# Kernel tuning notes

Measured on AMD Instinct MI355X. Metric: run time of the kernel, lower is better.

The kernel has to match this reference:

```python
import jax, jax.numpy as jnp
import numpy as np

N, E = 50000, 1600000
IN_DIM, HID, L, H = 300, 256, 3, 4
HD = HID // H  # 64
EPS = 1e-5


def setup_inputs() -> dict:
    key = jax.random.key(0)
    ks = jax.random.split(key, 24)
    s = 0.02
    inp = {
        'node_feats': jax.random.normal(ks[0], (N, IN_DIM), jnp.float32),
        'role': jax.random.randint(ks[1], (N,), 0, 3),
        'edge_src': jax.random.randint(ks[2], (E,), 0, N),
        'edge_dst': jax.random.randint(ks[3], (E,), 0, N),
        'edge_weights': jax.random.uniform(ks[4], (E,), jnp.float32),
        # input role transforms (question / entity / context)
        'Wq': jax.random.normal(ks[5], (IN_DIM, HID), jnp.float32) * s,
        'bq': jnp.zeros((HID,), jnp.float32),
        'We': jax.random.normal(ks[6], (IN_DIM, HID), jnp.float32) * s,
        'be': jnp.zeros((HID,), jnp.float32),
        'Wc': jax.random.normal(ks[7], (IN_DIM, HID), jnp.float32) * s,
        'bc': jnp.zeros((HID,), jnp.float32),
        # per-head value projections [H, HID, HD] (q/k projections omitted:
        # softmax over a scalar == 1.0, so they never affect output or grads)
        'Wv': jax.random.normal(ks[8], (H, HID, HD), jnp.float32) * s,
        'bv': jnp.zeros((H, HD), jnp.float32),
        # shared 'default' edge-type transform (the torch code always falls
        # through to 'default' because edata['rel'] entries are tensors)
        'Wd': jax.random.normal(ks[9], (HD, HD), jnp.float32) * s,
        'bd': jnp.zeros((HD,), jnp.float32),
        # attention_output
        'Wo': jax.random.normal(ks[10], (HID, HID), jnp.float32) * s,
        'bo': jnp.zeros((HID,), jnp.float32),
        # GRUCell params (torch layout: [3*HID, in], gate order r,z,n)
        'W_ih': jax.random.normal(ks[11], (3 * HID, HID), jnp.float32) * s,
        'W_hh': jax.random.normal(ks[12], (3 * HID, HID), jnp.float32) * s,
        'b_ih': jnp.zeros((3 * HID,), jnp.float32),
        'b_hh': jnp.zeros((3 * HID,), jnp.float32),
        # per-layer LayerNorm affine params [L, HID]
        'ln_w': jnp.ones((L, HID), jnp.float32),
        'ln_b': jnp.zeros((L, HID), jnp.float32),
    }
    return inp


def _layernorm(x, w, b):
    mu = jnp.mean(x, -1, keepdims=True)
    var = jnp.mean(jnp.square(x - mu), -1, keepdims=True)
    return (x - mu) * jax.lax.rsqrt(var + EPS) * w + b


def _gru_cell(x, hprev, W_ih, W_hh, b_ih, b_hh):
    gi = x @ W_ih.T + b_ih
    gh = hprev @ W_hh.T + b_hh
    i_r, i_z, i_n = jnp.split(gi, 3, axis=-1)
    h_r, h_z, h_n = jnp.split(gh, 3, axis=-1)
    r = jax.nn.sigmoid(i_r + h_r)
    z = jax.nn.sigmoid(i_z + h_z)
    n = jnp.tanh(i_n + r * h_n)
    return (1.0 - z) * n + z * hprev


def reference(node_feats, role, edge_src, edge_dst, edge_weights,
              Wq, bq, We, be, Wc, bc, Wv, bv, Wd, bd, Wo, bo,
              W_ih, W_hh, b_ih, b_hh, ln_w, ln_b):
    n_nodes = node_feats.shape[0]
    # role-dependent input transform: 0=question, 1=evidence/answer, 2=other
    hq = node_feats @ Wq + bq
    he = node_feats @ We + be
    hc = node_feats @ Wc + bc
    r = role[:, None]
    h = jax.nn.relu(jnp.where(r == 0, hq, jnp.where(r == 1, he, hc)))

    path_mem = jax.lax.stop_gradient(h)  # .detach().clone()
    prev_h = h
    num_layers, num_heads = ln_w.shape[0], Wv.shape[0]
    for layer in range(num_layers):
        head_msgs = []
        for hd in range(num_heads):
            # value proj + shared 'default' edge transform (node-level, fused)
            vt = (h @ Wv[hd] + bv[hd]) @ Wd + bd  # [N, HD]
            # scalar softmax == 1.0 -> attn_weight == edge_weight
            msg = vt[edge_src] * edge_weights[:, None]  # [E, HD]
            head_msgs.append(jax.ops.segment_sum(msg, edge_dst,
                                                 num_segments=n_nodes))
        combined = jnp.concatenate(head_msgs, axis=-1)  # [N, HID]
        path_mem = _gru_cell(combined, path_mem, W_ih, W_hh, b_ih, b_hh)
        h = _layernorm(prev_h + combined @ Wo + bo, ln_w[layer], ln_b[layer])
        # dropout: identity in eval mode
        prev_h = h
    return h + path_mem
```

## Files before the change

kernel.cpp:

```cpp
#include <hip/hip_runtime.h>
#include <math.h>

#define NN 50000
#define EE 1600000
#define IND 300
#define KPAD 320
#define NL 3
#define NBLK 785
#define AGG_NB 12500

typedef unsigned short u16;
typedef __attribute__((ext_vector_type(8))) short short8;
typedef __attribute__((ext_vector_type(4))) float floatx4;

__device__ __forceinline__ float b2f(u16 u) {
  union { unsigned i; float f; } v; v.i = ((unsigned)u) << 16; return v.f;
}
__device__ __forceinline__ u16 f2b(float f) {
  union { unsigned i; float f; } v; v.f = f;
  unsigned b = v.i; b += 0x7fffu + ((b >> 16) & 1u);
  return (u16)(b >> 16);
}
__device__ __forceinline__ float sigf(float x) { return 1.0f / (1.0f + __expf(-x)); }

__global__ void count_kernel(const int* __restrict__ dst, int* __restrict__ cnt) {
  int e = blockIdx.x * 256 + threadIdx.x;
  if (e < EE) atomicAdd(&cnt[dst[e]], 1);
}

__global__ __launch_bounds__(256) void scan1_kernel(const int* __restrict__ cnt,
                                                    int* __restrict__ rs,
                                                    int* __restrict__ bsum) {
  __shared__ int ws[4];
  const int t = threadIdx.x, l = t & 63, w = t >> 6;
  const int base = blockIdx.x * 2048 + t * 8;
  int v[8];
  int tot = 0;
  #pragma unroll
  for (int k = 0; k < 8; ++k) {
    int i = base + k;
    v[k] = (i < NN) ? cnt[i] : 0;
    tot += v[k];
  }
  int x = tot;
  #pragma unroll
  for (int off = 1; off < 64; off <<= 1) {
    int y = __shfl_up(x, off);
    if (l >= off) x += y;
  }
  if (l == 63) ws[w] = x;
  __syncthreads();
  int wpre = 0;
  for (int q = 0; q < w; ++q) wpre += ws[q];
  int run = wpre + (x - tot);
  #pragma unroll
  for (int k = 0; k < 8; ++k) {
    int i = base + k;
    if (i < NN) rs[i] = run;
    run += v[k];
  }
  if (t == 255) bsum[blockIdx.x] = wpre + x;
}

__global__ void scan2_kernel(int* __restrict__ bsum, int nb) {
  int l = threadIdx.x;
  int v = (l < nb) ? bsum[l] : 0;
  int x = v;
  #pragma unroll
  for (int off = 1; off < 64; off <<= 1) {
    int y = __shfl_up(x, off);
    if (l >= off) x += y;
  }
  if (l < nb) bsum[l] = x - v;
  if (l == 63) bsum[nb] = x;
}

__global__ void scan3_kernel(const int* __restrict__ bsum, int* __restrict__ rs, int nb) {
  int i = blockIdx.x * 256 + threadIdx.x;
  if (i < NN) rs[i] += bsum[i >> 11];
  if (i == 0) rs[NN] = bsum[nb];
}

__global__ void fill_kernel(const int* __restrict__ dst, const int* __restrict__ rs,
                            int* __restrict__ ncnt, const int* __restrict__ esrc,
                            const float* __restrict__ ew, int2* __restrict__ srcw) {
  int e = blockIdx.x * 256 + threadIdx.x;
  if (e < EE) {
    int d = dst[e];
    int p = atomicAdd(&ncnt[d], 1);
    int2 v;
    v.x = esrc[e];
    v.y = __float_as_int(ew[e]);
    srcw[rs[d] + p] = v;
  }
}

__global__ void role_count(const int* __restrict__ role, int* __restrict__ cnt3) {
  __shared__ int lc[3];
  if (threadIdx.x < 3) lc[threadIdx.x] = 0;
  __syncthreads();
  int i = blockIdx.x * 256 + threadIdx.x;
  if (i < NN) atomicAdd(&lc[role[i]], 1);
  __syncthreads();
  if (threadIdx.x < 3) atomicAdd(&cnt3[threadIdx.x], lc[threadIdx.x]);
}

__global__ void role_plan(const int* __restrict__ cnt3, int* __restrict__ pbase,
                          int* __restrict__ blkrole) {
  __shared__ int pb[4];
  if (threadIdx.x == 0) {
    pb[0] = 0;
    for (int b = 0; b < 3; ++b) pb[b + 1] = pb[b] + (((cnt3[b] + 63) >> 6) << 6);
    for (int b = 0; b < 4; ++b) pbase[b] = pb[b];
  }
  __syncthreads();
  for (int blk = threadIdx.x; blk < NBLK; blk += 256) {
    int m0 = blk * 64;
    int r = -1;
    for (int b = 0; b < 3; ++b)
      if (m0 >= pb[b] && m0 < pb[b + 1]) r = b;
    blkrole[blk] = r;
  }
}

__global__ void role_fill(const int* __restrict__ role, const int* __restrict__ pbase,
                          int* __restrict__ pos3, int* __restrict__ perm) {
  __shared__ int lcnt[3], lbase[3];
  int i = blockIdx.x * 256 + threadIdx.x;
  if (threadIdx.x < 3) lcnt[threadIdx.x] = 0;
  __syncthreads();
  int r = 0, lr = 0;
  bool valid = (i < NN);
  if (valid) {
    r = role[i];
    lr = atomicAdd(&lcnt[r], 1);
  }
  __syncthreads();
  if (threadIdx.x < 3) lbase[threadIdx.x] = atomicAdd(&pos3[threadIdx.x], lcnt[threadIdx.x]);
  __syncthreads();
  if (valid) perm[pbase[r] + lbase[r] + lr] = i;
}

__global__ void xcast_kernel(const float* __restrict__ X, u16* __restrict__ Xb) {
  size_t i = (size_t)blockIdx.x * 256 + threadIdx.x;
  if (i >= (size_t)NN * KPAD) return;
  int r = (int)(i / KPAD), k = (int)(i % KPAD);
  Xb[i] = (k < IND) ? f2b(X[(size_t)r * IND + k]) : (u16)0;
}

__global__ void wt3_kernel(const float* __restrict__ Wq, const float* __restrict__ We,
                           const float* __restrict__ Wc, u16* __restrict__ Wqt,
                           u16* __restrict__ Wet, u16* __restrict__ Wct) {
  int n = blockIdx.x;
  int which = blockIdx.y;
  const float* W = (which == 0) ? Wq : (which == 1) ? We : Wc;
  u16* Wt = (which == 0) ? Wqt : (which == 1) ? Wet : Wct;
  for (int k = threadIdx.x; k < KPAD; k += 256)
    Wt[(size_t)n * KPAD + k] = (k < IND) ? f2b(W[(size_t)k * 256 + n]) : (u16)0;
}

__global__ void wallt_kernel(const float* __restrict__ Wv, const float* __restrict__ Wd,
                             u16* __restrict__ Wallt) {
  int i = blockIdx.x;
  int c = threadIdx.x;
  int hd = c >> 6, j = c & 63;
  const float* wv = &Wv[hd * (256 * 64) + i * 64];
  float s = 0.f;
  #pragma unroll
  for (int m = 0; m < 64; ++m) s = fmaf(wv[m], Wd[m * 64 + j], s);
  Wallt[(size_t)c * 256 + i] = f2b(s);
}

__global__ void ball_kernel(const float* __restrict__ bv, const float* __restrict__ Wd,
                            const float* __restrict__ bd, float* __restrict__ ball) {
  int c = threadIdx.x;
  int hd = c >> 6, j = c & 63;
  float s = bd[j];
  #pragma unroll
  for (int m = 0; m < 64; ++m) s = fmaf(bv[hd * 64 + m], Wd[m * 64 + j], s);
  ball[c] = s;
}

__global__ void wot_kernel(const float* __restrict__ Wo, u16* __restrict__ Wot) {
  int n = blockIdx.x;
  int k = threadIdx.x;
  Wot[(size_t)n * 256 + k] = f2b(Wo[(size_t)k * 256 + n]);
}

__global__ void castbf2_kernel(const float* __restrict__ s0, const float* __restrict__ s1,
                               u16* __restrict__ d0, u16* __restrict__ d1) {
  int i = blockIdx.x * 256 + threadIdx.x;
  const int n = 768 * 256;
  if (i < n) d0[i] = f2b(s0[i]);
  else if (i < 2 * n) d1[i - n] = f2b(s1[i - n]);
}

#define GEMM_PROLOG \
  __shared__ __align__(16) u16 As[64][72]; \
  __shared__ __align__(16) u16 Bs[64][72]; \
  const int t = threadIdx.x; \
  const int lane = t & 63; \
  const int wv_ = t >> 6; \
  const int wr = wv_ >> 1, wc = wv_ & 1; \
  const int l15 = lane & 15, l4 = lane >> 4; \
  const int srow = t >> 2; \
  const int scol = (t & 3) << 4;

#define STAGE_A(AG, ASTRIDE, VALID, ROWIDX, K0) { \
  int4 v0 = {0, 0, 0, 0}, v1 = {0, 0, 0, 0}; \
  if (VALID) { \
    const int4* p_ = (const int4*)&(AG)[(size_t)(ROWIDX) * (ASTRIDE) + (K0) + scol]; \
    v0 = p_[0]; v1 = p_[1]; \
  } \
  *(int4*)&As[srow][scol] = v0; \
  *(int4*)&As[srow][scol + 8] = v1; }

#define STAGE_B(BG, BSTRIDE, ROWIDX, K0) { \
  const int4* p_ = (const int4*)&(BG)[(size_t)(ROWIDX) * (BSTRIDE) + (K0) + scol]; \
  *(int4*)&Bs[srow][scol] = p_[0]; \
  *(int4*)&Bs[srow][scol + 8] = p_[1]; }

#define MFMA_STEP(ACC) { \
  _Pragma("unroll") \
  for (int kc = 0; kc < 2; ++kc) { \
    short8 a0_ = *(const short8*)&As[wr * 32 + 0 + l15][kc * 32 + l4 * 8]; \
    short8 a1_ = *(const short8*)&As[wr * 32 + 16 + l15][kc * 32 + l4 * 8]; \
    short8 b0_ = *(const short8*)&Bs[wc * 32 + 0 + l15][kc * 32 + l4 * 8]; \
    short8 b1_ = *(const short8*)&Bs[wc * 32 + 16 + l15][kc * 32 + l4 * 8]; \
    ACC[0][0] = __builtin_amdgcn_mfma_f32_16x16x32_bf16(a0_, b0_, ACC[0][0], 0, 0, 0); \
    ACC[0][1] = __builtin_amdgcn_mfma_f32_16x16x32_bf16(a0_, b1_, ACC[0][1], 0, 0, 0); \
    ACC[1][0] = __builtin_amdgcn_mfma_f32_16x16x32_bf16(a1_, b0_, ACC[1][0], 0, 0, 0); \
    ACC[1][1] = __builtin_amdgcn_mfma_f32_16x16x32_bf16(a1_, b1_, ACC[1][1], 0, 0, 0); \
  } }

#define GEMM128_PROLOG \
  __shared__ __align__(16) u16 As[128][72]; \
  __shared__ __align__(16) u16 Bs[128][72]; \
  const int t = threadIdx.x; \
  const int lane = t & 63; \
  const int wv_ = t >> 6; \
  const int qr = (wv_ >> 1) * 64, qc = (wv_ & 1) * 64; \
  const int l15 = lane & 15, l4 = lane >> 4; \
  const int srow = t >> 1; \
  const int scol = (t & 1) * 32;

#define STAGE128_A(AG, ASTRIDE, VALID, ROWIDX, K0) { \
  int4 v0 = {0,0,0,0}, v1 = {0,0,0,0}, v2 = {0,0,0,0}, v3 = {0,0,0,0}; \
  if (VALID) { \
    const int4* p_ = (const int4*)&(AG)[(size_t)(ROWIDX) * (ASTRIDE) + (K0) + scol]; \
    v0 = p_[0]; v1 = p_[1]; v2 = p_[2]; v3 = p_[3]; \
  } \
  *(int4*)&As[srow][scol] = v0; *(int4*)&As[srow][scol + 8] = v1; \
  *(int4*)&As[srow][scol + 16] = v2; *(int4*)&As[srow][scol + 24] = v3; }

#define STAGE128_B(BG, BSTRIDE, ROWIDX, K0) { \
  const int4* p_ = (const int4*)&(BG)[(size_t)(ROWIDX) * (BSTRIDE) + (K0) + scol]; \
  *(int4*)&Bs[srow][scol] = p_[0]; *(int4*)&Bs[srow][scol + 8] = p_[1]; \
  *(int4*)&Bs[srow][scol + 16] = p_[2]; *(int4*)&Bs[srow][scol + 24] = p_[3]; }

#define MFMA128_STEP(ACC) { \
  _Pragma("unroll") \
  for (int kc = 0; kc < 2; ++kc) { \
    short8 af_[4], bf_[4]; \
    _Pragma("unroll") \
    for (int m = 0; m < 4; ++m) af_[m] = *(const short8*)&As[qr + m * 16 + l15][kc * 32 + l4 * 8]; \
    _Pragma("unroll") \
    for (int n = 0; n < 4; ++n) bf_[n] = *(const short8*)&Bs[qc + n * 16 + l15][kc * 32 + l4 * 8]; \
    _Pragma("unroll") \
    for (int m = 0; m < 4; ++m) \
      _Pragma("unroll") \
      for (int n = 0; n < 4; ++n) \
        ACC[m][n] = __builtin_amdgcn_mfma_f32_16x16x32_bf16(af_[m], bf_[n], ACC[m][n], 0, 0, 0); \
  } }

__global__ __launch_bounds__(256) void proj_mfma(
    const u16* __restrict__ Xb, const int* __restrict__ perm,
    const int* __restrict__ blkrole,
    const u16* __restrict__ Wqt, const u16* __restrict__ Wet, const u16* __restrict__ Wct,
    const float* __restrict__ bq, const float* __restrict__ be, const float* __restrict__ bc,
    u16* __restrict__ h, u16* __restrict__ pm) {
  const int brole = blkrole[blockIdx.y];
  if (brole < 0) return;
  GEMM_PROLOG
  const int m0 = blockIdx.y * 64;
  const int n0 = blockIdx.x * 64;
  const u16* Bt = (brole == 0) ? Wqt : (brole == 1) ? Wet : Wct;
  const float* bb = (brole == 0) ? bq : (brole == 1) ? be : bc;
  const int prow = perm[m0 + srow];
  floatx4 acc[2][2] = {};
  for (int k0 = 0; k0 < KPAD; k0 += 64) {
    STAGE_A(Xb, KPAD, prow >= 0, prow, k0)
    STAGE_B(Bt, KPAD, n0 + srow, k0)
    __syncthreads();
    MFMA_STEP(acc)
    __syncthreads();
  }
  #pragma unroll
  for (int m = 0; m < 2; ++m)
    #pragma unroll
    for (int reg = 0; reg < 4; ++reg) {
      int gr = m0 + wr * 32 + m * 16 + l4 * 4 + reg;
      int pr = perm[gr];
      if (pr >= 0) {
        #pragma unroll
        for (int n = 0; n < 2; ++n) {
          int c = n0 + wc * 32 + n * 16 + l15;
          float vo = fmaxf(acc[m][n][reg] + bb[c], 0.f);
          u16 ub = f2b(vo);
          h[(size_t)pr * 256 + c] = ub;
          pm[(size_t)pr * 256 + c] = ub;
        }
      }
    }
}

__global__ __launch_bounds__(256) void vgemm_mfma(
    const u16* __restrict__ A, const u16* __restrict__ Bt,
    const float* __restrict__ bias, u16* __restrict__ C) {
  GEMM128_PROLOG
  const int m0 = blockIdx.y * 128;
  const int n0 = blockIdx.x * 128;
  const int ar = m0 + srow;
  floatx4 acc[4][4] = {};
  for (int k0 = 0; k0 < 256; k0 += 64) {
    STAGE128_A(A, 256, ar < NN, ar, k0)
    STAGE128_B(Bt, 256, n0 + srow, k0)
    __syncthreads();
    MFMA128_STEP(acc)
    __syncthreads();
  }
  #pragma unroll
  for (int m = 0; m < 4; ++m)
    #pragma unroll
    for (int reg = 0; reg < 4; ++reg) {
      int gr = m0 + qr + m * 16 + l4 * 4 + reg;
      if (gr < NN) {
        #pragma unroll
        for (int n = 0; n < 4; ++n) {
          int c = n0 + qc + n * 16 + l15;
          C[(size_t)gr * 256 + c] = f2b(acc[m][n][reg] + bias[c]);
        }
      }
    }
}

__global__ __launch_bounds__(256) void agg_kernel(
    const int2* __restrict__ srcw, const int* __restrict__ rs,
    const u16* __restrict__ V, u16* __restrict__ comb) {
  int bid = blockIdx.x;
  int slice = (bid >= AGG_NB) ? 1 : 0;
  int nb = bid - slice * AGG_NB;
  int n = nb * 4 + (threadIdx.x >> 6);
  int l = threadIdx.x & 63;
  if (n >= NN) return;
  int s = rs[n], e = rs[n + 1];
  const size_t coff = (size_t)(slice << 7) + l * 2;
  float a0 = 0.f, a1 = 0.f, c0 = 0.f, c1 = 0.f;
  for (int base = s; base < e; base += 64) {
    int2 p = {0, 0};
    if (base + l < e) p = srcw[base + l];
    int cnt = min(64, e - base);
    int j = 0;
    for (; j + 4 <= cnt; j += 4) {
      int s0 = __shfl(p.x, j + 0), s1 = __shfl(p.x, j + 1);
      int s2 = __shfl(p.x, j + 2), s3 = __shfl(p.x, j + 3);
      float w0 = __int_as_float(__shfl(p.y, j + 0));
      float w1 = __int_as_float(__shfl(p.y, j + 1));
      float w2 = __int_as_float(__shfl(p.y, j + 2));
      float w3 = __int_as_float(__shfl(p.y, j + 3));
      ushort2 v0 = *(const ushort2*)&V[(size_t)s0 * 256 + coff];
      ushort2 v1 = *(const ushort2*)&V[(size_t)s1 * 256 + coff];
      ushort2 v2 = *(const ushort2*)&V[(size_t)s2 * 256 + coff];
      ushort2 v3 = *(const ushort2*)&V[(size_t)s3 * 256 + coff];
      a0 = fmaf(w0, b2f(v0.x), a0); a1 = fmaf(w0, b2f(v0.y), a1);
      c0 = fmaf(w1, b2f(v1.x), c0); c1 = fmaf(w1, b2f(v1.y), c1);
      a0 = fmaf(w2, b2f(v2.x), a0); a1 = fmaf(w2, b2f(v2.y), a1);
      c0 = fmaf(w3, b2f(v3.x), c0); c1 = fmaf(w3, b2f(v3.y), c1);
    }
    for (; j < cnt; ++j) {
      int src = __shfl(p.x, j);
      float w = __int_as_float(__shfl(p.y, j));
      ushort2 v = *(const ushort2*)&V[(size_t)src * 256 + coff];
      a0 = fmaf(w, b2f(v.x), a0); a1 = fmaf(w, b2f(v.y), a1);
    }
  }
  a0 += c0; a1 += c1;
  ushort2 o;
  o.x = f2b(a0); o.y = f2b(a1);
  *(ushort2*)&comb[(size_t)n * 256 + coff] = o;
}

__global__ __launch_bounds__(256) void gru_mfma(
    const u16* __restrict__ comb, const u16* __restrict__ pmc,
    const u16* __restrict__ Wiht, const u16* __restrict__ Whht,
    const float* __restrict__ bih, const float* __restrict__ bhh,
    u16* __restrict__ pmn) {
  __shared__ __align__(16) u16 As[2][64][40];
  __shared__ __align__(16) u16 Bs[6][64][40];
  const int t = threadIdx.x;
  const int lane = t & 63;
  const int wv_ = t >> 6;
  const int wr = wv_ >> 1, wc = wv_ & 1;
  const int l15 = lane & 15, l4 = lane >> 4;
  const int srow = t >> 2;
  const int kq = (t & 3) << 3;
  const int m0 = blockIdx.y * 64;
  const int cb = blockIdx.x;
  const int ar = m0 + srow;
  const bool av = ar < NN;
  floatx4 acc[6][2][2] = {};
  for (int k0 = 0; k0 < 256; k0 += 32) {
    {
      int4 v0 = {0, 0, 0, 0}, u0 = {0, 0, 0, 0};
      if (av) {
        v0 = *(const int4*)&comb[(size_t)ar * 256 + k0 + kq];
        u0 = *(const int4*)&pmc[(size_t)ar * 256 + k0 + kq];
      }
      *(int4*)&As[0][srow][kq] = v0;
      *(int4*)&As[1][srow][kq] = u0;
    }
    #pragma unroll
    for (int g = 0; g < 3; ++g) {
      size_t row = (size_t)(g * 256 + cb * 64 + srow);
      *(int4*)&Bs[g][srow][kq] = *(const int4*)&Wiht[row * 256 + k0 + kq];
      *(int4*)&Bs[3 + g][srow][kq] = *(const int4*)&Whht[row * 256 + k0 + kq];
    }
    __syncthreads();
    short8 a0f[2], a1f[2];
    #pragma unroll
    for (int m = 0; m < 2; ++m) {
      a0f[m] = *(const short8*)&As[0][wr * 32 + m * 16 + l15][l4 * 8];
      a1f[m] = *(const short8*)&As[1][wr * 32 + m * 16 + l15][l4 * 8];
    }
    #pragma unroll
    for (int g = 0; g < 3; ++g) {
      short8 b0 = *(const short8*)&Bs[g][wc * 32 + 0 + l15][l4 * 8];
      short8 b1 = *(const short8*)&Bs[g][wc * 32 + 16 + l15][l4 * 8];
      acc[g][0][0] = __builtin_amdgcn_mfma_f32_16x16x32_bf16(a0f[0], b0, acc[g][0][0], 0, 0, 0);
      acc[g][0][1] = __builtin_amdgcn_mfma_f32_16x16x32_bf16(a0f[0], b1, acc[g][0][1], 0, 0, 0);
      acc[g][1][0] = __builtin_amdgcn_mfma_f32_16x16x32_bf16(a0f[1], b0, acc[g][1][0], 0, 0, 0);
      acc[g][1][1] = __builtin_amdgcn_mfma_f32_16x16x32_bf16(a0f[1], b1, acc[g][1][1], 0, 0, 0);
    }
    #pragma unroll
    for (int g = 3; g < 6; ++g) {
      short8 b0 = *(const short8*)&Bs[g][wc * 32 + 0 + l15][l4 * 8];
      short8 b1 = *(const short8*)&Bs[g][wc * 32 + 16 + l15][l4 * 8];
      acc[g][0][0] = __builtin_amdgcn_mfma_f32_16x16x32_bf16(a1f[0], b0, acc[g][0][0], 0, 0, 0);
      acc[g][0][1] = __builtin_amdgcn_mfma_f32_16x16x32_bf16(a1f[0], b1, acc[g][0][1], 0, 0, 0);
      acc[g][1][0] = __builtin_amdgcn_mfma_f32_16x16x32_bf16(a1f[1], b0, acc[g][1][0], 0, 0, 0);
      acc[g][1][1] = __builtin_amdgcn_mfma_f32_16x16x32_bf16(a1f[1], b1, acc[g][1][1], 0, 0, 0);
    }
    __syncthreads();
  }
  #pragma unroll
  for (int m = 0; m < 2; ++m)
    #pragma unroll
    for (int reg = 0; reg < 4; ++reg) {
      int gr = m0 + wr * 32 + m * 16 + l4 * 4 + reg;
      if (gr < NN) {
        #pragma unroll
        for (int n = 0; n < 2; ++n) {
          int c = cb * 64 + wc * 32 + n * 16 + l15;
          float r = sigf(acc[0][m][n][reg] + acc[3][m][n][reg] + bih[c] + bhh[c]);
          float z = sigf(acc[1][m][n][reg] + acc[4][m][n][reg] + bih[256 + c] + bhh[256 + c]);
          float i_n = acc[2][m][n][reg] + bih[512 + c];
          float h_n = acc[5][m][n][reg] + bhh[512 + c];
          float nn2 = tanhf(i_n + r * h_n);
          float po = b2f(pmc[(size_t)gr * 256 + c]);
          pmn[(size_t)gr * 256 + c] = f2b((1.f - z) * nn2 + z * po);
        }
      }
    }
}

__global__ __launch_bounds__(256) void wo_ln_mfma(
    const u16* __restrict__ comb, const u16* __restrict__ Wot,
    const float* __restrict__ bo, const u16* __restrict__ h_in,
    const float* __restrict__ lnw, const float* __restrict__ lnb,
    u16* __restrict__ h_out, const u16* __restrict__ pm,
    float* __restrict__ out, int last) {
  __shared__ __align__(16) u16 As[64][72];
  __shared__ __align__(16) u16 Bs[256][72];
  __shared__ float2 red[64][4];
  const int t = threadIdx.x;
  const int lane = t & 63;
  const int w = t >> 6;
  const int l15 = lane & 15, l4 = lane >> 4;
  const int m0 = blockIdx.x * 64;
  const int arow = t >> 2;
  const int ascol = (t & 3) << 4;
  floatx4 acc[4][4] = {};
  for (int k0 = 0; k0 < 256; k0 += 64) {
    {
      int r = m0 + arow;
      int4 v0 = {0, 0, 0, 0}, v1 = {0, 0, 0, 0};
      if (r < NN) {
        const int4* p = (const int4*)&comb[(size_t)r * 256 + k0 + ascol];
        v0 = p[0]; v1 = p[1];
      }
      *(int4*)&As[arow][ascol] = v0;
      *(int4*)&As[arow][ascol + 8] = v1;
    }
    {
      const int4* p = (const int4*)&Wot[(size_t)t * 256 + k0];
      #pragma unroll
      for (int q = 0; q < 8; ++q) *(int4*)&Bs[t][q * 8] = p[q];
    }
    __syncthreads();
    #pragma unroll
    for (int kc = 0; kc < 2; ++kc) {
      short8 af[4], bf[4];
      #pragma unroll
      for (int m = 0; m < 4; ++m) af[m] = *(const short8*)&As[m * 16 + l15][kc * 32 + l4 * 8];
      #pragma unroll
      for (int n = 0; n < 4; ++n) bf[n] = *(const short8*)&Bs[w * 64 + n * 16 + l15][kc * 32 + l4 * 8];
      #pragma unroll
      for (int m = 0; m < 4; ++m)
        #pragma unroll
        for (int n = 0; n < 4; ++n)
          acc[m][n] = __builtin_amdgcn_mfma_f32_16x16x32_bf16(af[m], bf[n], acc[m][n], 0, 0, 0);
    }
    __syncthreads();
  }
  #pragma unroll
  for (int m = 0; m < 4; ++m)
    #pragma unroll
    for (int reg = 0; reg < 4; ++reg) {
      int rloc = m * 16 + l4 * 4 + reg;
      int gr = m0 + rloc;
      float s = 0.f, s2 = 0.f;
      #pragma unroll
      for (int n = 0; n < 4; ++n) {
        int c = w * 64 + n * 16 + l15;
        float hv = (gr < NN) ? b2f(h_in[(size_t)gr * 256 + c]) : 0.f;
        float v = acc[m][n][reg] + bo[c] + hv;
        acc[m][n][reg] = v;
        s += v;
        s2 = fmaf(v, v, s2);
      }
      #pragma unroll
      for (int off = 1; off < 16; off <<= 1) {
        s += __shfl_xor(s, off);
        s2 += __shfl_xor(s2, off);
      }
      if (l15 == 0) red[rloc][w] = make_float2(s, s2);
    }
  __syncthreads();
  #pragma unroll
  for (int m = 0; m < 4; ++m)
    #pragma unroll
    for (int reg = 0; reg < 4; ++reg) {
      int rloc = m * 16 + l4 * 4 + reg;
      int gr = m0 + rloc;
      float2 r0 = red[rloc][0], r1 = red[rloc][1], r2 = red[rloc][2], r3 = red[rloc][3];
      float tot = (r0.x + r1.x) + (r2.x + r3.x);
      float tot2 = (r0.y + r1.y) + (r2.y + r3.y);
      float mu = tot * (1.f / 256.f);
      float var = tot2 * (1.f / 256.f) - mu * mu;
      float inv = rsqrtf(fmaxf(var, 0.f) + 1e-5f);
      if (gr < NN) {
        #pragma unroll
        for (int n = 0; n < 4; ++n) {
          int c = w * 64 + n * 16 + l15;
          float lnv = (acc[m][n][reg] - mu) * inv * lnw[c] + lnb[c];
          if (last) {
            out[(size_t)gr * 256 + c] = b2f(f2b(lnv)) + b2f(pm[(size_t)gr * 256 + c]);
          } else {
            h_out[(size_t)gr * 256 + c] = f2b(lnv);
          }
        }
      }
    }
}

extern "C" void kernel_launch(void* const* d_in, const int* in_sizes, int n_in,
                              void* d_out, int out_size, void* d_ws, size_t ws_size,
                              hipStream_t stream) {
  const float* node_feats = (const float*)d_in[0];
  const int* role = (const int*)d_in[1];
  const int* esrc = (const int*)d_in[2];
  const int* edst = (const int*)d_in[3];
  const float* ew = (const float*)d_in[4];
  const float* Wq = (const float*)d_in[5];
  const float* bq = (const float*)d_in[6];
  const float* We = (const float*)d_in[7];
  const float* be = (const float*)d_in[8];
  const float* Wc = (const float*)d_in[9];
  const float* bc = (const float*)d_in[10];
  const float* Wv = (const float*)d_in[11];
  const float* bv = (const float*)d_in[12];
  const float* Wd = (const float*)d_in[13];
  const float* bd = (const float*)d_in[14];
  const float* Wo = (const float*)d_in[15];
  const float* bo = (const float*)d_in[16];
  const float* Wih = (const float*)d_in[17];
  const float* Whh = (const float*)d_in[18];
  const float* bih = (const float*)d_in[19];
  const float* bhh = (const float*)d_in[20];
  const float* lnw = (const float*)d_in[21];
  const float* lnb = (const float*)d_in[22];
  float* out = (float*)d_out;

  char* ws = (char*)d_ws;
  size_t off = 0;
  auto take = [&](size_t bytes) {
    char* p = ws + off;
    off = (off + bytes + 511) & ~(size_t)511;
    return p;
  };
  const size_t NC2 = (size_t)NN * 256 * 2;
  u16* Xb = (u16*)take((size_t)NN * KPAD * 2);
  u16* h = (u16*)take(NC2);
  u16* pm0 = (u16*)take(NC2);
  u16* pm1 = (u16*)take(NC2);
  u16* V = (u16*)take(NC2);
  u16* comb = (u16*)take(NC2);
  u16* Wqt = (u16*)take((size_t)256 * KPAD * 2);
  u16* Wet = (u16*)take((size_t)256 * KPAD * 2);
  u16* Wct = (u16*)take((size_t)256 * KPAD * 2);
  u16* Wallt = (u16*)take((size_t)256 * 256 * 2);
  u16* Wot = (u16*)take((size_t)256 * 256 * 2);
  u16* Wiht = (u16*)take((size_t)768 * 256 * 2);
  u16* Whht = (u16*)take((size_t)768 * 256 * 2);
  float* ball = (float*)take(256 * 4);
  int* cnt = (int*)take((size_t)NN * 4);
  int* rs = (int*)take((size_t)(NN + 1) * 4);
  int* ncnt = (int*)take((size_t)NN * 4);
  int2* srcw = (int2*)take((size_t)EE * 8);
  int* cnt3 = (int*)take(16);
  int* pos3 = (int*)take(16);
  int* pbase = (int*)take(16);
  int* blkrole = (int*)take((size_t)NBLK * 4);
  int* perm = (int*)take((size_t)NBLK * 64 * 4);
  int* bsum = (int*)take(64 * 4);

  const int NB_SCAN = (NN + 2047) / 2048;

  hipMemsetAsync(cnt, 0, (size_t)NN * 4, stream);
  hipMemsetAsync(ncnt, 0, (size_t)NN * 4, stream);
  hipMemsetAsync(cnt3, 0, 16, stream);
  hipMemsetAsync(pos3, 0, 16, stream);
  hipMemsetAsync(perm, 0xFF, (size_t)NBLK * 64 * 4, stream);

  count_kernel<<<(EE + 255) / 256, 256, 0, stream>>>(edst, cnt);
  scan1_kernel<<<NB_SCAN, 256, 0, stream>>>(cnt, rs, bsum);
  scan2_kernel<<<1, 64, 0, stream>>>(bsum, NB_SCAN);
  scan3_kernel<<<(NN + 255) / 256, 256, 0, stream>>>(bsum, rs, NB_SCAN);
  fill_kernel<<<(EE + 255) / 256, 256, 0, stream>>>(edst, rs, ncnt, esrc, ew, srcw);

  role_count<<<(NN + 255) / 256, 256, 0, stream>>>(role, cnt3);
  role_plan<<<1, 256, 0, stream>>>(cnt3, pbase, blkrole);
  role_fill<<<(NN + 255) / 256, 256, 0, stream>>>(role, pbase, pos3, perm);

  xcast_kernel<<<(int)(((size_t)NN * KPAD + 255) / 256), 256, 0, stream>>>(node_feats, Xb);
  wt3_kernel<<<dim3(256, 3), 256, 0, stream>>>(Wq, We, Wc, Wqt, Wet, Wct);
  wallt_kernel<<<256, 256, 0, stream>>>(Wv, Wd, Wallt);
  ball_kernel<<<1, 256, 0, stream>>>(bv, Wd, bd, ball);
  wot_kernel<<<256, 256, 0, stream>>>(Wo, Wot);
  castbf2_kernel<<<(2 * 768 * 256 + 255) / 256, 256, 0, stream>>>(Wih, Whh, Wiht, Whht);

  proj_mfma<<<dim3(4, NBLK), 256, 0, stream>>>(Xb, perm, blkrole, Wqt, Wet, Wct,
                                               bq, be, bc, h, pm0);

  u16* pmc = pm0;
  u16* pmn = pm1;
  const int MB128 = (NN + 127) / 128;
  const int MB64 = (NN + 63) / 64;
  for (int layer = 0; layer < NL; ++layer) {
    vgemm_mfma<<<dim3(2, MB128), 256, 0, stream>>>(h, Wallt, ball, V);
    agg_kernel<<<2 * AGG_NB, 256, 0, stream>>>(srcw, rs, V, comb);
    gru_mfma<<<dim3(4, MB64), 256, 0, stream>>>(comb, pmc, Wiht, Whht, bih, bhh, pmn);
    wo_ln_mfma<<<MB64, 256, 0, stream>>>(comb, Wot, bo, h,
                                         lnw + layer * 256, lnb + layer * 256,
                                         h, pmn, out, (layer == NL - 1) ? 1 : 0);
    u16* sw = pmc; pmc = pmn; pmn = sw;
  }
}
```

Baseline: 1.169 ms.

## Slice V into 32-column slabs, pack edge metadata, widen GRU K-tile

The value GEMM now writes V as eight column-major slabs of 32 columns. Aggregation then runs over eight column slices, each gathering from a much smaller slab that can stay cache-resident, with half-waves processing alternating edges through shared-memory metadata. Edge source and weight are packed into one u32 (16-bit source index, bf16 weight), which halves the metadata footprint but rounds the weights to bf16 and relies on N < 65536. Metadata is now re-read once per slice, eight times in total. The GRU GEMM also doubles its K tile to 64 to halve the number of barriers.

```diff
diff --git a/kernel.cpp b/kernel.cpp
--- a/kernel.cpp
+++ b/kernel.cpp
@@ -10,6 +10,7 @@
 #define AGG_NB 12500
 
 typedef unsigned short u16;
+typedef unsigned int u32;
 typedef __attribute__((ext_vector_type(8))) short short8;
 typedef __attribute__((ext_vector_type(4))) float floatx4;
 
@@ -83,14 +84,12 @@
 
 __global__ void fill_kernel(const int* __restrict__ dst, const int* __restrict__ rs,
                             int* __restrict__ ncnt, const int* __restrict__ esrc,
-                            const float* __restrict__ ew, int2* __restrict__ srcw) {
+                            const float* __restrict__ ew, u32* __restrict__ srcw) {
   int e = blockIdx.x * 256 + threadIdx.x;
   if (e < EE) {
     int d = dst[e];
     int p = atomicAdd(&ncnt[d], 1);
-    int2 v;
-    v.x = esrc[e];
-    v.y = __float_as_int(ew[e]);
+    u32 v = ((u32)f2b(ew[e]) << 16) | (u32)esrc[e];
     srcw[rs[d] + p] = v;
   }
 }
@@ -316,7 +315,7 @@
 
 __global__ __launch_bounds__(256) void vgemm_mfma(
     const u16* __restrict__ A, const u16* __restrict__ Bt,
-    const float* __restrict__ bias, u16* __restrict__ C) {
+    const float* __restrict__ bias, u16* __restrict__ Vs) {
   GEMM128_PROLOG
   const int m0 = blockIdx.y * 128;
   const int n0 = blockIdx.x * 128;
@@ -338,56 +337,53 @@
         #pragma unroll
         for (int n = 0; n < 4; ++n) {
           int c = n0 + qc + n * 16 + l15;
-          C[(size_t)gr * 256 + c] = f2b(acc[m][n][reg] + bias[c]);
+          size_t off = ((size_t)(c >> 5) * NN + gr) * 32 + (c & 31);
+          Vs[off] = f2b(acc[m][n][reg] + bias[c]);
         }
       }
     }
 }
 
 __global__ __launch_bounds__(256) void agg_kernel(
-    const int2* __restrict__ srcw, const int* __restrict__ rs,
-    const u16* __restrict__ V, u16* __restrict__ comb) {
+    const u32* __restrict__ srcw, const int* __restrict__ rs,
+    const u16* __restrict__ Vs, u16* __restrict__ comb) {
+  __shared__ u32 meta[4][64];
   int bid = blockIdx.x;
-  int slice = (bid >= AGG_NB) ? 1 : 0;
+  int slice = bid / AGG_NB;
   int nb = bid - slice * AGG_NB;
-  int n = nb * 4 + (threadIdx.x >> 6);
-  int l = threadIdx.x & 63;
-  if (n >= NN) return;
+  int wid = threadIdx.x >> 6;
+  int n = nb * 4 + wid;
+  int lane = threadIdx.x & 63;
+  int hh = lane >> 5;
+  int u = lane & 31;
   int s = rs[n], e = rs[n + 1];
-  const size_t coff = (size_t)(slice << 7) + l * 2;
-  float a0 = 0.f, a1 = 0.f, c0 = 0.f, c1 = 0.f;
+  const u16* __restrict__ vbase = Vs + (size_t)slice * NN * 32;
+  float a0 = 0.f, a1 = 0.f, a2 = 0.f, a3 = 0.f;
   for (int base = s; base < e; base += 64) {
-    int2 p = {0, 0};
-    if (base + l < e) p = srcw[base + l];
+    u32 m = 0;
+    if (base + lane < e) m = srcw[base + lane];
+    meta[wid][lane] = m;
     int cnt = min(64, e - base);
-    int j = 0;
-    for (; j + 4 <= cnt; j += 4) {
-      int s0 = __shfl(p.x, j + 0), s1 = __shfl(p.x, j + 1);
-      int s2 = __shfl(p.x, j + 2), s3 = __shfl(p.x, j + 3);
-      float w0 = __int_as_float(__shfl(p.y, j + 0));
-      float w1 = __int_as_float(__shfl(p.y, j + 1));
-      float w2 = __int_as_float(__shfl(p.y, j + 2));
-      float w3 = __int_as_float(__shfl(p.y, j + 3));
-      ushort2 v0 = *(const ushort2*)&V[(size_t)s0 * 256 + coff];
-      ushort2 v1 = *(const ushort2*)&V[(size_t)s1 * 256 + coff];
-      ushort2 v2 = *(const ushort2*)&V[(size_t)s2 * 256 + coff];
-      ushort2 v3 = *(const ushort2*)&V[(size_t)s3 * 256 + coff];
-      a0 = fmaf(w0, b2f(v0.x), a0); a1 = fmaf(w0, b2f(v0.y), a1);
-      c0 = fmaf(w1, b2f(v1.x), c0); c1 = fmaf(w1, b2f(v1.y), c1);
-      a0 = fmaf(w2, b2f(v2.x), a0); a1 = fmaf(w2, b2f(v2.y), a1);
-      c0 = fmaf(w3, b2f(v3.x), c0); c1 = fmaf(w3, b2f(v3.y), c1);
-    }
-    for (; j < cnt; ++j) {
-      int src = __shfl(p.x, j);
-      float w = __int_as_float(__shfl(p.y, j));
-      ushort2 v = *(const ushort2*)&V[(size_t)src * 256 + coff];
-      a0 = fmaf(w, b2f(v.x), a0); a1 = fmaf(w, b2f(v.y), a1);
-    }
-  }
-  a0 += c0; a1 += c1;
-  ushort2 o;
-  o.x = f2b(a0); o.y = f2b(a1);
-  *(ushort2*)&comb[(size_t)n * 256 + coff] = o;
+    for (int k = 0; k < cnt; k += 8) {
+      u32 m0 = meta[wid][k + hh];
+      u32 m1 = meta[wid][k + 2 + hh];
+      u32 m2 = meta[wid][k + 4 + hh];
+      u32 m3 = meta[wid][k + 6 + hh];
+      float w0 = __int_as_float((int)(m0 & 0xffff0000u));
+      float w1 = __int_as_float((int)(m1 & 0xffff0000u));
+      float w2 = __int_as_float((int)(m2 & 0xffff0000u));
+      float w3 = __int_as_float((int)(m3 & 0xffff0000u));
+      float f0 = b2f(vbase[(size_t)(m0 & 0xffffu) * 32 + u]);
+      float f1 = b2f(vbase[(size_t)(m1 & 0xffffu) * 32 + u]);
+      float f2 = b2f(vbase[(size_t)(m2 & 0xffffu) * 32 + u]);
+      float f3 = b2f(vbase[(size_t)(m3 & 0xffffu) * 32 + u]);
+      a0 = fmaf(w0, f0, a0); a1 = fmaf(w1, f1, a1);
+      a2 = fmaf(w2, f2, a2); a3 = fmaf(w3, f3, a3);
+    }
+  }
+  float a = (a0 + a1) + (a2 + a3);
+  a += __shfl_xor(a, 32);
+  if (hh == 0) comb[(size_t)n * 256 + slice * 32 + u] = f2b(a);
 }
 
 __global__ __launch_bounds__(256) void gru_mfma(
@@ -395,60 +391,69 @@
     const u16* __restrict__ Wiht, const u16* __restrict__ Whht,
     const float* __restrict__ bih, const float* __restrict__ bhh,
     u16* __restrict__ pmn) {
-  __shared__ __align__(16) u16 As[2][64][40];
-  __shared__ __align__(16) u16 Bs[6][64][40];
+  __shared__ __align__(16) u16 As[2][64][72];
+  __shared__ __align__(16) u16 Bs[6][64][72];
   const int t = threadIdx.x;
   const int lane = t & 63;
   const int wv_ = t >> 6;
   const int wr = wv_ >> 1, wc = wv_ & 1;
   const int l15 = lane & 15, l4 = lane >> 4;
   const int srow = t >> 2;
-  const int kq = (t & 3) << 3;
+  const int scol = (t & 3) << 4;
   const int m0 = blockIdx.y * 64;
   const int cb = blockIdx.x;
   const int ar = m0 + srow;
   const bool av = ar < NN;
   floatx4 acc[6][2][2] = {};
-  for (int k0 = 0; k0 < 256; k0 += 32) {
+  for (int k0 = 0; k0 < 256; k0 += 64) {
     {
-      int4 v0 = {0, 0, 0, 0}, u0 = {0, 0, 0, 0};
+      int4 v0 = {0,0,0,0}, v1 = {0,0,0,0}, u0 = {0,0,0,0}, u1 = {0,0,0,0};
       if (av) {
-        v0 = *(const int4*)&comb[(size_t)ar * 256 + k0 + kq];
-        u0 = *(const int4*)&pmc[(size_t)ar * 256 + k0 + kq];
-      }
-      *(int4*)&As[0][srow][kq] = v0;
-      *(int4*)&As[1][srow][kq] = u0;
+        const int4* pa = (const int4*)&comb[(size_t)ar * 256 + k0 + scol];
+        v0 = pa[0]; v1 = pa[1];
+        const int4* pb = (const int4*)&pmc[(size_t)ar * 256 + k0 + scol];
+        u0 = pb[0]; u1 = pb[1];
+      }
+      *(int4*)&As[0][srow][scol] = v0; *(int4*)&As[0][srow][scol + 8] = v1;
+      *(int4*)&As[1][srow][scol] = u0; *(int4*)&As[1][srow][scol + 8] = u1;
     }
     #pragma unroll
     for (int g = 0; g < 3; ++g) {
       size_t row = (size_t)(g * 256 + cb * 64 + srow);
-      *(int4*)&Bs[g][srow][kq] = *(const int4*)&Wiht[row * 256 + k0 + kq];
-      *(int4*)&Bs[3 + g][srow][kq] = *(const int4*)&Whht[row * 256 + k0 + kq];
-    }
-    __syncthreads();
-    short8 a0f[2], a1f[2];
-    #pragma unroll
-    for (int m = 0; m < 2; ++m) {
-      a0f[m] = *(const short8*)&As[0][wr * 32 + m * 16 + l15][l4 * 8];
-      a1f[m] = *(const short8*)&As[1][wr * 32 + m * 16 + l15][l4 * 8];
-    }
-    #pragma unroll
-    for (int g = 0; g < 3; ++g) {
-      short8 b0 = *(const short8*)&Bs[g][wc * 32 + 0 + l15][l4 * 8];
-      short8 b1 = *(const short8*)&Bs[g][wc * 32 + 16 + l15][l4 * 8];
-      acc[g][0][0] = __builtin_amdgcn_mfma_f32_16x16x32_bf16(a0f[0], b0, acc[g][0][0], 0, 0, 0);
-      acc[g][0][1] = __builtin_amdgcn_mfma_f32_16x16x32_bf16(a0f[0], b1, acc[g][0][1], 0, 0, 0);
-      acc[g][1][0] = __builtin_amdgcn_mfma_f32_16x16x32_bf16(a0f[1], b0, acc[g][1][0], 0, 0, 0);
-      acc[g][1][1] = __builtin_amdgcn_mfma_f32_16x16x32_bf16(a0f[1], b1, acc[g][1][1], 0, 0, 0);
-    }
-    #pragma unroll
-    for (int g = 3; g < 6; ++g) {
-      short8 b0 = *(const short8*)&Bs[g][wc * 32 + 0 + l15][l4 * 8];
-      short8 b1 = *(const short8*)&Bs[g][wc * 32 + 16 + l15][l4 * 8];
-      acc[g][0][0] = __builtin_amdgcn_mfma_f32_16x16x32_bf16(a1f[0], b0, acc[g][0][0], 0, 0, 0);
-      acc[g][0][1] = __builtin_amdgcn_mfma_f32_16x16x32_bf16(a1f[0], b1, acc[g][0][1], 0, 0, 0);
-      acc[g][1][0] = __builtin_amdgcn_mfma_f32_16x16x32_bf16(a1f[1], b0, acc[g][1][0], 0, 0, 0);
-      acc[g][1][1] = __builtin_amdgcn_mfma_f32_16x16x32_bf16(a1f[1], b1, acc[g][1][1], 0, 0, 0);
+      const int4* p1 = (const int4*)&Wiht[row * 256 + k0 + scol];
+      *(int4*)&Bs[g][srow][scol] = p1[0];
+      *(int4*)&Bs[g][srow][scol + 8] = p1[1];
+      const int4* p2 = (const int4*)&Whht[row * 256 + k0 + scol];
+      *(int4*)&Bs[3 + g][srow][scol] = p2[0];
+      *(int4*)&Bs[3 + g][srow][scol + 8] = p2[1];
+    }
+    __syncthreads();
+    #pragma unroll
+    for (int kc = 0; kc < 2; ++kc) {
+      short8 a0f[2], a1f[2];
+      #pragma unroll
+      for (int m = 0; m < 2; ++m) {
+        a0f[m] = *(const short8*)&As[0][wr * 32 + m * 16 + l15][kc * 32 + l4 * 8];
+        a1f[m] = *(const short8*)&As[1][wr * 32 + m * 16 + l15][kc * 32 + l4 * 8];
+      }
+      #pragma unroll
+      for (int g = 0; g < 3; ++g) {
+        short8 b0 = *(const short8*)&Bs[g][wc * 32 + 0 + l15][kc * 32 + l4 * 8];
+        short8 b1 = *(const short8*)&Bs[g][wc * 32 + 16 + l15][kc * 32 + l4 * 8];
+        acc[g][0][0] = __builtin_amdgcn_mfma_f32_16x16x32_bf16(a0f[0], b0, acc[g][0][0], 0, 0, 0);
+        acc[g][0][1] = __builtin_amdgcn_mfma_f32_16x16x32_bf16(a0f[0], b1, acc[g][0][1], 0, 0, 0);
+        acc[g][1][0] = __builtin_amdgcn_mfma_f32_16x16x32_bf16(a0f[1], b0, acc[g][1][0], 0, 0, 0);
+        acc[g][1][1] = __builtin_amdgcn_mfma_f32_16x16x32_bf16(a0f[1], b1, acc[g][1][1], 0, 0, 0);
+      }
+      #pragma unroll
+      for (int g = 3; g < 6; ++g) {
+        short8 b0 = *(const short8*)&Bs[g][wc * 32 + 0 + l15][kc * 32 + l4 * 8];
+        short8 b1 = *(const short8*)&Bs[g][wc * 32 + 16 + l15][kc * 32 + l4 * 8];
+        acc[g][0][0] = __builtin_amdgcn_mfma_f32_16x16x32_bf16(a1f[0], b0, acc[g][0][0], 0, 0, 0);
+        acc[g][0][1] = __builtin_amdgcn_mfma_f32_16x16x32_bf16(a1f[0], b1, acc[g][0][1], 0, 0, 0);
+        acc[g][1][0] = __builtin_amdgcn_mfma_f32_16x16x32_bf16(a1f[1], b0, acc[g][1][0], 0, 0, 0);
+        acc[g][1][1] = __builtin_amdgcn_mfma_f32_16x16x32_bf16(a1f[1], b1, acc[g][1][1], 0, 0, 0);
+      }
     }
     __syncthreads();
   }
@@ -613,7 +618,7 @@
   u16* h = (u16*)take(NC2);
   u16* pm0 = (u16*)take(NC2);
   u16* pm1 = (u16*)take(NC2);
-  u16* V = (u16*)take(NC2);
+  u16* Vs = (u16*)take(NC2);
   u16* comb = (u16*)take(NC2);
   u16* Wqt = (u16*)take((size_t)256 * KPAD * 2);
   u16* Wet = (u16*)take((size_t)256 * KPAD * 2);
@@ -626,7 +631,7 @@
   int* cnt = (int*)take((size_t)NN * 4);
   int* rs = (int*)take((size_t)(NN + 1) * 4);
   int* ncnt = (int*)take((size_t)NN * 4);
-  int2* srcw = (int2*)take((size_t)EE * 8);
+  u32* srcw = (u32*)take((size_t)EE * 4);
   int* cnt3 = (int*)take(16);
   int* pos3 = (int*)take(16);
   int* pbase = (int*)take(16);
@@ -667,8 +672,8 @@
   const int MB128 = (NN + 127) / 128;
   const int MB64 = (NN + 63) / 64;
   for (int layer = 0; layer < NL; ++layer) {
-    vgemm_mfma<<<dim3(2, MB128), 256, 0, stream>>>(h, Wallt, ball, V);
-    agg_kernel<<<2 * AGG_NB, 256, 0, stream>>>(srcw, rs, V, comb);
+    vgemm_mfma<<<dim3(2, MB128), 256, 0, stream>>>(h, Wallt, ball, Vs);
+    agg_kernel<<<8 * AGG_NB, 256, 0, stream>>>(srcw, rs, Vs, comb);
     gru_mfma<<<dim3(4, MB64), 256, 0, stream>>>(comb, pmc, Wiht, Whht, bih, bhh, pmn);
     wo_ln_mfma<<<MB64, 256, 0, stream>>>(comb, Wot, bo, h,
                                          lnw + layer * 256, lnb + layer * 256,
```

Result: slower. 1.289 ms (+10.3%).
